# Kernel optimization log

Hardware: AMD Instinct MI355X
Metric: run time of the kernel (lower is better)

## Reference

```python
import jax, jax.numpy as jnp
import numpy as np

# dims
B, T, H = 4, 2048, 768
HEADS, D = 4, 768          # GATConv(out_channels=768, heads=4, concat=False)
L = 3                      # num_layers
WIN = 2
K = 2 * WIN + 1
EPS = 1e-5
NEG_SLOPE = 0.2            # PyG GATConv leaky_relu slope


def setup_inputs() -> dict:
    key = jax.random.key(0)
    ks = jax.random.split(key, 4)
    s = 1.0 / np.sqrt(H)
    x = jax.random.normal(ks[0], (B, T, H), jnp.float32)
    W = jax.random.normal(ks[1], (L, H, HEADS, D), jnp.float32) * s   # lin weights per layer
    a_src = jax.random.normal(ks[2], (L, HEADS, D), jnp.float32) * s  # att_src
    a_dst = jax.random.normal(ks[3], (L, HEADS, D), jnp.float32) * s  # att_dst
    bias = jnp.zeros((L, D), jnp.float32)                             # GATConv bias (concat=False -> [D])
    gamma = jnp.ones((L, H), jnp.float32)                             # LayerNorm weight
    beta = jnp.zeros((L, H), jnp.float32)                             # LayerNorm bias
    return {"x": x, "W": W, "a_src": a_src, "a_dst": a_dst,
            "bias": bias, "gamma": gamma, "beta": beta}


def _layernorm(z, g, b):
    m = jnp.mean(z, axis=-1, keepdims=True)
    v = jnp.mean((z - m) ** 2, axis=-1, keepdims=True)
    return (z - m) * jax.lax.rsqrt(v + EPS) * g + b


def _gat_layer(x, Wl, asrc_w, adst_w, bias_l, idx, mask):
    # x: [B,T,H]; banded GAT with neighborhoods idx: [T,K] (clipped), mask: [T,K]
    h = jnp.einsum('bti,ihd->bthd', x, Wl)                 # [B,T,heads,D]
    asrc = jnp.einsum('bthd,hd->bth', h, asrc_w)           # per-source-node score term
    adst = jnp.einsum('bthd,hd->bth', h, adst_w)           # per-target-node score term
    h_nb = h[:, idx]                                       # [B,T,K,heads,D] gathered neighbors j
    score = jax.nn.leaky_relu(asrc[:, idx] + adst[:, :, None, :], NEG_SLOPE)  # [B,T,K,heads]
    score = jnp.where(mask[None, :, :, None], score, -jnp.inf)
    attn = jax.nn.softmax(score, axis=2)                   # softmax over incoming edges per target
    out = jnp.einsum('btkh,btkhd->bthd', attn, h_nb)       # weighted aggregation
    return out.mean(axis=2) + bias_l                       # concat=False -> mean over heads


def reference(x, W, a_src, a_dst, bias, gamma, beta):
    # banded neighborhood indices (window edges both directions + self-loop from PyG default)
    offs = jnp.arange(-WIN, WIN + 1)
    idx = jnp.arange(T)[:, None] + offs[None, :]           # [T,K]
    mask = (idx >= 0) & (idx < T)
    idx = jnp.clip(idx, 0, T - 1)
    for l in range(L):
        res = x
        y = _gat_layer(x, W[l], a_src[l], a_dst[l], bias[l], idx, mask)
        x = _layernorm(y + res, gamma[l], beta[l])         # dropout = identity in eval
    return x
```

## Files before the change

kernel.cpp:

```cpp
#include <hip/hip_runtime.h>
#include <stdint.h>

#define TT 2048
#define BB 4
#define HH 768
#define NHEADS 4
#define DD 768
#define NN 3072
#define LL 3
#define BT 8192
#define KNB 5
#define NBLK 12
#define ATPB 4
#define NROWS 8

typedef __bf16 bf16x8 __attribute__((ext_vector_type(8)));
typedef float f32x4 __attribute__((ext_vector_type(4)));

__device__ __forceinline__ unsigned short f2bf(float f){
  union { float f; unsigned u; } v; v.f = f;
  unsigned u = v.u;
  return (unsigned short)((u + 0x7FFFu + ((u >> 16) & 1u)) >> 16);
}
__device__ __forceinline__ float bf2f(unsigned short h){
  union { unsigned u; float f; } v; v.u = ((unsigned)h) << 16;
  return v.f;
}
__device__ __forceinline__ void gload16(const unsigned short* g, unsigned short* l){
  __builtin_amdgcn_global_load_lds((const __attribute__((address_space(1))) void*)g,
                                   (__attribute__((address_space(3))) void*)l, 16, 0, 0);
}

__global__ void wt_kernel(const float* __restrict__ W, unsigned short* __restrict__ Wt){
  __shared__ float tile[32][33];
  int l = blockIdx.z;
  int n0 = blockIdx.x * 32, k0 = blockIdx.y * 32;
  int tx = threadIdx.x, ty = threadIdx.y;
  const float* Wl = W + (size_t)l * HH * NN;
  for (int r = 0; r < 4; r++)
    tile[ty + r*8][tx] = Wl[(size_t)(k0 + ty + r*8) * NN + n0 + tx];
  __syncthreads();
  unsigned short* Wtl = Wt + (size_t)l * NN * HH;
  for (int r = 0; r < 4; r++){
    int n = n0 + ty + r*8;
    Wtl[(size_t)n * HH + k0 + tx] = f2bf(tile[tx][ty + r*8]);
  }
}

__global__ void xconv_kernel(const float* __restrict__ x, unsigned short* __restrict__ xb){
  int i = blockIdx.x * blockDim.x + threadIdx.x;
  float4 v = ((const float4*)x)[i];
  ushort4 o;
  o.x = f2bf(v.x); o.y = f2bf(v.y); o.z = f2bf(v.z); o.w = f2bf(v.w);
  *(ushort4*)(xb + (size_t)i * 4) = o;
}

#define BM 128
#define BN 128
#define BK 64

__global__ __launch_bounds__(256, 3) void gemm_kernel(
    const unsigned short* __restrict__ xb,
    const unsigned short* __restrict__ wt,
    unsigned short* __restrict__ hout,
    const float* __restrict__ a_srcl,
    const float* __restrict__ a_dstl,
    float* __restrict__ psrc,
    float* __restrict__ pdst){
  __shared__ __align__(16) unsigned short xs[BM][BK];
  __shared__ __align__(16) unsigned short wsd[BN][BK];
  int id = blockIdx.x;
  int xcd = id & 7;
  int s = id >> 3;
  int bn_i = s / 8;
  int bm_i = (s & 7) + xcd * 8;
  int bm = bm_i * BM;
  int bn = bn_i * BN;
  int tid = threadIdx.x;
  int wave = tid >> 6, lane = tid & 63;
  int m16 = lane & 15, q = lane >> 4;
  int wm = (wave >> 1) * 64, wn = (wave & 1) * 64;
  int r8 = lane >> 3, c8 = lane & 7;
  int cg = (c8 ^ r8) * 8;
  const unsigned short* ga[4]; const unsigned short* gb[4];
  unsigned short* la[4]; unsigned short* lb[4];
  #pragma unroll
  for (int ss = 0; ss < 4; ss++){
    int row = wave * 32 + ss * 8;
    ga[ss] = xb + (size_t)(bm + row + r8) * HH + cg;
    gb[ss] = wt + (size_t)(bn + row + r8) * HH + cg;
    la[ss] = &xs[row][0];
    lb[ss] = &wsd[row][0];
  }
  int rd0 = ((0 + q) ^ (m16 & 7)) * 8;
  int rd1 = ((4 + q) ^ (m16 & 7)) * 8;
  f32x4 acc[4][4] = {};
  for (int k0 = 0; k0 < HH; k0 += BK){
    #pragma unroll
    for (int ss = 0; ss < 4; ss++){
      gload16(ga[ss] + k0, la[ss]);
      gload16(gb[ss] + k0, lb[ss]);
    }
    __syncthreads();
    bf16x8 af[4], bfr[4];
    for (int i = 0; i < 4; i++)
      af[i] = __builtin_bit_cast(bf16x8, *(const uint4*)(&xs[wm + i*16 + m16][rd0]));
    for (int j = 0; j < 4; j++)
      bfr[j] = __builtin_bit_cast(bf16x8, *(const uint4*)(&wsd[wn + j*16 + m16][rd0]));
    for (int i = 0; i < 4; i++)
      for (int j = 0; j < 4; j++)
        acc[i][j] = __builtin_amdgcn_mfma_f32_16x16x32_bf16(af[i], bfr[j], acc[i][j], 0, 0, 0);
    for (int i = 0; i < 4; i++)
      af[i] = __builtin_bit_cast(bf16x8, *(const uint4*)(&xs[wm + i*16 + m16][rd1]));
    for (int j = 0; j < 4; j++)
      bfr[j] = __builtin_bit_cast(bf16x8, *(const uint4*)(&wsd[wn + j*16 + m16][rd1]));
    for (int i = 0; i < 4; i++)
      for (int j = 0; j < 4; j++)
        acc[i][j] = __builtin_amdgcn_mfma_f32_16x16x32_bf16(af[i], bfr[j], acc[i][j], 0, 0, 0);
    __syncthreads();
  }
  for (int i = 0; i < 4; i++){
    int row0 = bm + wm + i*16 + q*4;
    for (int j = 0; j < 4; j++){
      int col = bn + wn + j*16 + m16;
      unsigned short* hp = hout + (size_t)row0 * NN + col;
      hp[0]            = f2bf(acc[i][j][0]);
      hp[NN]           = f2bf(acc[i][j][1]);
      hp[2*(size_t)NN] = f2bf(acc[i][j][2]);
      hp[3*(size_t)NN] = f2bf(acc[i][j][3]);
    }
  }
  int col0 = bn + wn;
  int head = col0 / DD;
  int blk  = (col0 % DD) >> 6;
  float wsrc[4], wdstw[4];
  for (int j = 0; j < 4; j++){
    int n = col0 + j*16 + m16;
    wsrc[j]  = a_srcl[n];
    wdstw[j] = a_dstl[n];
  }
  for (int i = 0; i < 4; i++){
    for (int reg = 0; reg < 4; reg++){
      float ss = 0.f, dd = 0.f;
      for (int j = 0; j < 4; j++){
        float v = acc[i][j][reg];
        ss += v * wsrc[j];
        dd += v * wdstw[j];
      }
      ss += __shfl_xor(ss, 1, 64); dd += __shfl_xor(dd, 1, 64);
      ss += __shfl_xor(ss, 2, 64); dd += __shfl_xor(dd, 2, 64);
      ss += __shfl_xor(ss, 4, 64); dd += __shfl_xor(dd, 4, 64);
      ss += __shfl_xor(ss, 8, 64); dd += __shfl_xor(dd, 8, 64);
      if (m16 == 0){
        int row = bm + wm + i*16 + q*4 + reg;
        size_t slot = (size_t)row * (NHEADS * NBLK) + head * NBLK + blk;
        psrc[slot] = ss;
        pdst[slot] = dd;
      }
    }
  }
}

__global__ __launch_bounds__(384) void attn_ln_kernel(const unsigned short* __restrict__ h,
    const float* __restrict__ psrc, const float* __restrict__ pdst,
    const float* __restrict__ xin_f32,
    const unsigned short* __restrict__ xin_bf,
    const float* __restrict__ bias_l,
    const float* __restrict__ gamma_l, const float* __restrict__ beta_l,
    float* __restrict__ x_out, unsigned short* __restrict__ xb_next,
    int write_f32){
  int bid = blockIdx.x;
  int grp = ((bid & 7) << 8) | (bid >> 3);
  int token0 = grp * ATPB;
  int t0 = token0 & (TT - 1);
  int bseq = token0 >> 11;
  int tid = threadIdx.x;
  int wave = tid >> 6, lane = tid & 63;
  int ti = tid / 96, c = tid % 96;
  int token = token0 + ti;
  __shared__ float as_sh[NROWS * NHEADS], ad_sh[NROWS * NHEADS];
  __shared__ float part_s[ATPB * 96], part_q[ATPB * 96];
  __shared__ float mv_mean[ATPB], mv_rstd[ATPB];

  if (tid < 2 * NROWS * NHEADS){
    int which = tid >= NROWS * NHEADS;
    int i = tid & (NROWS * NHEADS - 1);
    int lt = i >> 2, head = i & 3;
    int tcl = min(max(t0 - 2 + lt, 0), TT - 1);
    const float* p = (which ? pdst : psrc) +
        ((size_t)(bseq * TT + tcl) * NHEADS + head) * NBLK;
    float4 a = *(const float4*)(p);
    float4 b = *(const float4*)(p + 4);
    float4 d = *(const float4*)(p + 8);
    float s = a.x+a.y+a.z+a.w + b.x+b.y+b.z+b.w + d.x+d.y+d.z+d.w;
    (which ? ad_sh : as_sh)[i] = s;
  }

  float xr[8], bb[8], gr[8], br[8];
  if (xin_f32){
    const float4* p = (const float4*)&xin_f32[(size_t)token * HH + c * 8];
    *(float4*)&xr[0] = p[0]; *(float4*)&xr[4] = p[1];
  } else {
    uint4 u = *(const uint4*)&xin_bf[(size_t)token * HH + c * 8];
    const unsigned short* us = (const unsigned short*)&u;
    #pragma unroll
    for (int e = 0; e < 8; e++) xr[e] = bf2f(us[e]);
  }
  { const float4* p = (const float4*)&bias_l[c * 8];
    *(float4*)&bb[0] = p[0]; *(float4*)&bb[4] = p[1]; }
  { const float4* p = (const float4*)&gamma_l[c * 8];
    *(float4*)&gr[0] = p[0]; *(float4*)&gr[4] = p[1]; }
  { const float4* p = (const float4*)&beta_l[c * 8];
    *(float4*)&br[0] = p[0]; *(float4*)&br[4] = p[1]; }
  __syncthreads();

  float aw[NHEADS][KNB];
  #pragma unroll
  for (int hd = 0; hd < NHEADS; hd++){
    float ad = ad_sh[(ti + 2) * NHEADS + hd];
    float sc[KNB];
    float mx = -3.0e38f;
    #pragma unroll
    for (int k = 0; k < KNB; k++){
      int tn = t0 + ti + k - 2;
      if (tn >= 0 && tn < TT){
        float s = as_sh[(ti + k) * NHEADS + hd] + ad;
        s = s > 0.f ? s : 0.2f * s;
        sc[k] = s; mx = fmaxf(mx, s);
      } else sc[k] = -3.0e38f;
    }
    float den = 0.f;
    #pragma unroll
    for (int k = 0; k < KNB; k++){
      float e = (sc[k] > -1.0e38f) ? __expf(sc[k] - mx) : 0.f;
      sc[k] = e; den += e;
    }
    float inv = 0.25f / den;
    #pragma unroll
    for (int k = 0; k < KNB; k++) aw[hd][k] = sc[k] * inv;
  }

  const unsigned short* hbase = h + (size_t)(bseq * TT) * NN + c * 8;
  float y8[8] = {};
  #pragma unroll
  for (int k = 0; k < KNB; k++){
    int g = t0 + ti + k - 2;
    g = min(max(g, 0), TT - 1);
    const unsigned short* hr = hbase + (size_t)g * NN;
    #pragma unroll
    for (int hd = 0; hd < NHEADS; hd++){
      bf16x8 v = __builtin_bit_cast(bf16x8, *(const uint4*)(hr + hd * DD));
      float a = aw[hd][k];
      #pragma unroll
      for (int e = 0; e < 8; e++) y8[e] += a * (float)v[e];
    }
  }
  float s = 0.f, sq = 0.f;
  #pragma unroll
  for (int e = 0; e < 8; e++){
    float zz = y8[e] + bb[e] + xr[e];
    y8[e] = zz; s += zz; sq += zz * zz;
  }
  part_s[tid] = s; part_q[tid] = sq;
  __syncthreads();
  if (wave < ATPB){
    float vs = part_s[wave * 96 + lane];
    float vq = part_q[wave * 96 + lane];
    if (lane < 32){
      vs += part_s[wave * 96 + 64 + lane];
      vq += part_q[wave * 96 + 64 + lane];
    }
    for (int off = 32; off > 0; off >>= 1){
      vs += __shfl_xor(vs, off, 64);
      vq += __shfl_xor(vq, off, 64);
    }
    if (lane == 0){
      float mean = vs * (1.f / HH);
      float var = vq * (1.f / HH) - mean * mean;
      mv_mean[wave] = mean;
      mv_rstd[wave] = rsqrtf(var + 1e-5f);
    }
  }
  __syncthreads();
  float mean = mv_mean[ti], rstd = mv_rstd[ti];
  float o[8];
  #pragma unroll
  for (int e = 0; e < 8; e++)
    o[e] = (y8[e] - mean) * rstd * gr[e] + br[e];
  if (write_f32){
    float* xo = &x_out[(size_t)token * HH + c * 8];
    *(float4*)&xo[0] = *(float4*)&o[0];
    *(float4*)&xo[4] = *(float4*)&o[4];
  } else {
    unsigned short o16[8];
    #pragma unroll
    for (int e = 0; e < 8; e++) o16[e] = f2bf(o[e]);
    *(uint4*)(&xb_next[(size_t)token * HH + c * 8]) = *(uint4*)&o16[0];
  }
}

extern "C" void kernel_launch(void* const* d_in, const int* in_sizes, int n_in,
                              void* d_out, int out_size, void* d_ws, size_t ws_size,
                              hipStream_t stream) {
  const float* x     = (const float*)d_in[0];
  const float* W     = (const float*)d_in[1];
  const float* a_src = (const float*)d_in[2];
  const float* a_dst = (const float*)d_in[3];
  const float* bias  = (const float*)d_in[4];
  const float* gamma = (const float*)d_in[5];
  const float* beta  = (const float*)d_in[6];
  float* out = (float*)d_out;

  char* ws = (char*)d_ws;
  size_t off = 0;
  auto alloc = [&](size_t bytes)->char*{
    char* p = ws + off;
    off = (off + bytes + 255) & ~(size_t)255;
    return p;
  };
  unsigned short* wt   = (unsigned short*)alloc((size_t)LL * NN * HH * 2);
  unsigned short* xb   = (unsigned short*)alloc((size_t)BT * HH * 2);
  unsigned short* hbuf = (unsigned short*)alloc((size_t)BT * NN * 2);
  float* psrc  = (float*)alloc((size_t)BT * NHEADS * NBLK * 4);
  float* pdst  = (float*)alloc((size_t)BT * NHEADS * NBLK * 4);

  wt_kernel<<<dim3(NN/32, HH/32, LL), dim3(32, 8), 0, stream>>>(W, wt);
  xconv_kernel<<<(BT * HH / 4) / 256, 256, 0, stream>>>(x, xb);

  for (int l = 0; l < LL; l++){
    gemm_kernel<<<(NN / BN) * (BT / BM), 256, 0, stream>>>(
        xb, wt + (size_t)l * NN * HH, hbuf,
        a_src + (size_t)l * NHEADS * DD, a_dst + (size_t)l * NHEADS * DD,
        psrc, pdst);
    attn_ln_kernel<<<BT / ATPB, 384, 0, stream>>>(hbuf, psrc, pdst,
        (l == 0) ? x : nullptr, xb,
        bias + (size_t)l * DD, gamma + (size_t)l * HH, beta + (size_t)l * HH,
        out, xb, (l == LL - 1) ? 1 : 0);
  }
}
```

Measured before the change: 339.5 us.

## Restructure attention+LayerNorm kernel to one wave per token with shuffles

The attention/LayerNorm kernel now assigns one 64-lane wave per token (8 tokens per 512-thread block) instead of 96 threads per token across waves. Score partial sums are loaded by lanes and broadcast with shuffles, and the LayerNorm reduction is done fully in-wave, which removes all shared memory and __syncthreads. Each lane handles 12 elements with 8-byte loads instead of 16-byte loads, which may lower memory access efficiency.

```diff
diff --git a/kernel.cpp b/kernel.cpp
--- a/kernel.cpp
+++ b/kernel.cpp
@@ -11,8 +11,6 @@
 #define BT 8192
 #define KNB 5
 #define NBLK 12
-#define ATPB 4
-#define NROWS 8
 
 typedef __bf16 bf16x8 __attribute__((ext_vector_type(8)));
 typedef float f32x4 __attribute__((ext_vector_type(4)));
@@ -161,7 +159,7 @@
   }
 }
 
-__global__ __launch_bounds__(384) void attn_ln_kernel(const unsigned short* __restrict__ h,
+__global__ __launch_bounds__(512) void attn_ln_kernel(const unsigned short* __restrict__ h,
     const float* __restrict__ psrc, const float* __restrict__ pdst,
     const float* __restrict__ xin_f32,
     const unsigned short* __restrict__ xin_bf,
@@ -170,61 +168,41 @@
     float* __restrict__ x_out, unsigned short* __restrict__ xb_next,
     int write_f32){
   int bid = blockIdx.x;
-  int grp = ((bid & 7) << 8) | (bid >> 3);
-  int token0 = grp * ATPB;
-  int t0 = token0 & (TT - 1);
-  int bseq = token0 >> 11;
-  int tid = threadIdx.x;
-  int wave = tid >> 6, lane = tid & 63;
-  int ti = tid / 96, c = tid % 96;
-  int token = token0 + ti;
-  __shared__ float as_sh[NROWS * NHEADS], ad_sh[NROWS * NHEADS];
-  __shared__ float part_s[ATPB * 96], part_q[ATPB * 96];
-  __shared__ float mv_mean[ATPB], mv_rstd[ATPB];
-
-  if (tid < 2 * NROWS * NHEADS){
-    int which = tid >= NROWS * NHEADS;
-    int i = tid & (NROWS * NHEADS - 1);
-    int lt = i >> 2, head = i & 3;
-    int tcl = min(max(t0 - 2 + lt, 0), TT - 1);
-    const float* p = (which ? pdst : psrc) +
-        ((size_t)(bseq * TT + tcl) * NHEADS + head) * NBLK;
+  int grp = ((bid & 7) << 7) | (bid >> 3);
+  int wave = threadIdx.x >> 6, lane = threadIdx.x & 63;
+  int token = grp * 8 + wave;
+  int t = token & (TT - 1);
+  int bseq = token >> 11;
+
+  float red = 0.f;
+  if (lane < 24){
+    const float* p;
+    if (lane < 20){
+      int k = lane >> 2, hd = lane & 3;
+      int row = min(max(t - 2 + k, 0), TT - 1);
+      p = psrc + ((size_t)(bseq * TT + row) * NHEADS + hd) * NBLK;
+    } else {
+      int hd = lane - 20;
+      p = pdst + ((size_t)(bseq * TT + t) * NHEADS + hd) * NBLK;
+    }
     float4 a = *(const float4*)(p);
     float4 b = *(const float4*)(p + 4);
     float4 d = *(const float4*)(p + 8);
-    float s = a.x+a.y+a.z+a.w + b.x+b.y+b.z+b.w + d.x+d.y+d.z+d.w;
-    (which ? ad_sh : as_sh)[i] = s;
-  }
-
-  float xr[8], bb[8], gr[8], br[8];
-  if (xin_f32){
-    const float4* p = (const float4*)&xin_f32[(size_t)token * HH + c * 8];
-    *(float4*)&xr[0] = p[0]; *(float4*)&xr[4] = p[1];
-  } else {
-    uint4 u = *(const uint4*)&xin_bf[(size_t)token * HH + c * 8];
-    const unsigned short* us = (const unsigned short*)&u;
-    #pragma unroll
-    for (int e = 0; e < 8; e++) xr[e] = bf2f(us[e]);
-  }
-  { const float4* p = (const float4*)&bias_l[c * 8];
-    *(float4*)&bb[0] = p[0]; *(float4*)&bb[4] = p[1]; }
-  { const float4* p = (const float4*)&gamma_l[c * 8];
-    *(float4*)&gr[0] = p[0]; *(float4*)&gr[4] = p[1]; }
-  { const float4* p = (const float4*)&beta_l[c * 8];
-    *(float4*)&br[0] = p[0]; *(float4*)&br[4] = p[1]; }
-  __syncthreads();
-
-  float aw[NHEADS][KNB];
+    red = a.x+a.y+a.z+a.w + b.x+b.y+b.z+b.w + d.x+d.y+d.z+d.w;
+  }
+
+  const unsigned short* hb = h + (size_t)(bseq * TT) * NN + lane * 4;
+  float y[12] = {};
   #pragma unroll
   for (int hd = 0; hd < NHEADS; hd++){
-    float ad = ad_sh[(ti + 2) * NHEADS + hd];
+    float ad = __shfl(red, 20 + hd, 64);
     float sc[KNB];
     float mx = -3.0e38f;
     #pragma unroll
     for (int k = 0; k < KNB; k++){
-      int tn = t0 + ti + k - 2;
+      int tn = t + k - 2;
       if (tn >= 0 && tn < TT){
-        float s = as_sh[(ti + k) * NHEADS + hd] + ad;
+        float s = __shfl(red, k * 4 + hd, 64) + ad;
         s = s > 0.f ? s : 0.2f * s;
         sc[k] = s; mx = fmaxf(mx, s);
       } else sc[k] = -3.0e38f;
@@ -237,65 +215,82 @@
     }
     float inv = 0.25f / den;
     #pragma unroll
-    for (int k = 0; k < KNB; k++) aw[hd][k] = sc[k] * inv;
-  }
-
-  const unsigned short* hbase = h + (size_t)(bseq * TT) * NN + c * 8;
-  float y8[8] = {};
-  #pragma unroll
-  for (int k = 0; k < KNB; k++){
-    int g = t0 + ti + k - 2;
-    g = min(max(g, 0), TT - 1);
-    const unsigned short* hr = hbase + (size_t)g * NN;
-    #pragma unroll
-    for (int hd = 0; hd < NHEADS; hd++){
-      bf16x8 v = __builtin_bit_cast(bf16x8, *(const uint4*)(hr + hd * DD));
-      float a = aw[hd][k];
+    for (int k = 0; k < KNB; k++){
+      int g = t + k - 2;
+      g = min(max(g, 0), TT - 1);
+      const unsigned short* hr = hb + (size_t)g * NN + hd * DD;
+      float a = sc[k] * inv;
       #pragma unroll
-      for (int e = 0; e < 8; e++) y8[e] += a * (float)v[e];
-    }
-  }
+      for (int j = 0; j < 3; j++){
+        uint2 u = *(const uint2*)(hr + j * 256);
+        const unsigned short* us = (const unsigned short*)&u;
+        y[j*4+0] += a * bf2f(us[0]);
+        y[j*4+1] += a * bf2f(us[1]);
+        y[j*4+2] += a * bf2f(us[2]);
+        y[j*4+3] += a * bf2f(us[3]);
+      }
+    }
+  }
+
+  float xr[12], bb[12];
+  if (xin_f32){
+    const float* xp = xin_f32 + (size_t)token * HH + lane * 4;
+    #pragma unroll
+    for (int j = 0; j < 3; j++) *(float4*)&xr[j*4] = *(const float4*)(xp + j * 256);
+  } else {
+    const unsigned short* xp = xin_bf + (size_t)token * HH + lane * 4;
+    #pragma unroll
+    for (int j = 0; j < 3; j++){
+      uint2 u = *(const uint2*)(xp + j * 256);
+      const unsigned short* us = (const unsigned short*)&u;
+      xr[j*4+0] = bf2f(us[0]); xr[j*4+1] = bf2f(us[1]);
+      xr[j*4+2] = bf2f(us[2]); xr[j*4+3] = bf2f(us[3]);
+    }
+  }
+  { const float* p = bias_l + lane * 4;
+    #pragma unroll
+    for (int j = 0; j < 3; j++) *(float4*)&bb[j*4] = *(const float4*)(p + j * 256); }
   float s = 0.f, sq = 0.f;
   #pragma unroll
-  for (int e = 0; e < 8; e++){
-    float zz = y8[e] + bb[e] + xr[e];
-    y8[e] = zz; s += zz; sq += zz * zz;
-  }
-  part_s[tid] = s; part_q[tid] = sq;
-  __syncthreads();
-  if (wave < ATPB){
-    float vs = part_s[wave * 96 + lane];
-    float vq = part_q[wave * 96 + lane];
-    if (lane < 32){
-      vs += part_s[wave * 96 + 64 + lane];
-      vq += part_q[wave * 96 + 64 + lane];
-    }
-    for (int off = 32; off > 0; off >>= 1){
-      vs += __shfl_xor(vs, off, 64);
-      vq += __shfl_xor(vq, off, 64);
-    }
-    if (lane == 0){
-      float mean = vs * (1.f / HH);
-      float var = vq * (1.f / HH) - mean * mean;
-      mv_mean[wave] = mean;
-      mv_rstd[wave] = rsqrtf(var + 1e-5f);
-    }
-  }
-  __syncthreads();
-  float mean = mv_mean[ti], rstd = mv_rstd[ti];
-  float o[8];
-  #pragma unroll
-  for (int e = 0; e < 8; e++)
-    o[e] = (y8[e] - mean) * rstd * gr[e] + br[e];
+  for (int e = 0; e < 12; e++){
+    float zz = y[e] + bb[e] + xr[e];
+    y[e] = zz; s += zz; sq += zz * zz;
+  }
+  #pragma unroll
+  for (int off = 32; off > 0; off >>= 1){
+    s  += __shfl_xor(s, off, 64);
+    sq += __shfl_xor(sq, off, 64);
+  }
+  float mean = s * (1.f / HH);
+  float var = sq * (1.f / HH) - mean * mean;
+  float rstd = rsqrtf(var + 1e-5f);
+
+  float gr[12], br[12];
+  { const float* p = gamma_l + lane * 4;
+    #pragma unroll
+    for (int j = 0; j < 3; j++) *(float4*)&gr[j*4] = *(const float4*)(p + j * 256); }
+  { const float* p = beta_l + lane * 4;
+    #pragma unroll
+    for (int j = 0; j < 3; j++) *(float4*)&br[j*4] = *(const float4*)(p + j * 256); }
+
+  float o[12];
+  #pragma unroll
+  for (int e = 0; e < 12; e++)
+    o[e] = (y[e] - mean) * rstd * gr[e] + br[e];
+
   if (write_f32){
-    float* xo = &x_out[(size_t)token * HH + c * 8];
-    *(float4*)&xo[0] = *(float4*)&o[0];
-    *(float4*)&xo[4] = *(float4*)&o[4];
+    float* xo = x_out + (size_t)token * HH + lane * 4;
+    #pragma unroll
+    for (int j = 0; j < 3; j++) *(float4*)(xo + j * 256) = *(float4*)&o[j*4];
   } else {
-    unsigned short o16[8];
-    #pragma unroll
-    for (int e = 0; e < 8; e++) o16[e] = f2bf(o[e]);
-    *(uint4*)(&xb_next[(size_t)token * HH + c * 8]) = *(uint4*)&o16[0];
+    unsigned short* xo = xb_next + (size_t)token * HH + lane * 4;
+    #pragma unroll
+    for (int j = 0; j < 3; j++){
+      ushort4 o16;
+      o16.x = f2bf(o[j*4+0]); o16.y = f2bf(o[j*4+1]);
+      o16.z = f2bf(o[j*4+2]); o16.w = f2bf(o[j*4+3]);
+      *(ushort4*)(xo + j * 256) = o16;
+    }
   }
 }
 
@@ -332,7 +327,7 @@
         xb, wt + (size_t)l * NN * HH, hbuf,
         a_src + (size_t)l * NHEADS * DD, a_dst + (size_t)l * NHEADS * DD,
         psrc, pdst);
-    attn_ln_kernel<<<BT / ATPB, 384, 0, stream>>>(hbuf, psrc, pdst,
+    attn_ln_kernel<<<BT / 8, 512, 0, stream>>>(hbuf, psrc, pdst,
         (l == 0) ? x : nullptr, xb,
         bias + (size_t)l * DD, gamma + (size_t)l * HH, beta + (size_t)l * HH,
         out, xb, (l == LL - 1) ? 1 : 0);
```

New measurement: 324.6 us. 4.4% less time.
